# Optimization experiments

Hardware: AMD Instinct MI355X
Metric: run time of the kernel (lower is better)

The kernel has to match this reference:

```python
import jax, jax.numpy as jnp
import numpy as np

NEG_SLOPE = 0.2  # PyG GATConv default negative_slope


def setup_inputs() -> dict:
    key = jax.random.key(0)
    k1, k2, k3, k4, k5 = jax.random.split(key, 5)
    N, E, IN, H, C = 50000, 800000, 128, 4, 64
    x = jax.random.normal(k1, (N, IN), dtype=jnp.float32)
    edge_index = jax.random.randint(k2, (2, E), 0, N, dtype=jnp.int32)
    W = jax.random.normal(k3, (IN, H * C), dtype=jnp.float32) * (1.0 / np.sqrt(IN))
    att_src = jax.random.normal(k4, (H, C), dtype=jnp.float32) * 0.1
    att_dst = jax.random.normal(k5, (H, C), dtype=jnp.float32) * 0.1
    bias = jnp.zeros((C,), dtype=jnp.float32)
    return {"x": x, "edge_index": edge_index, "W": W,
            "att_src": att_src, "att_dst": att_dst, "bias": bias}


def reference(x, edge_index, W, att_src, att_dst, bias):
    N = x.shape[0]
    H, C = att_src.shape
    # add self loops (PyG GATConv default add_self_loops=True)
    loop = jnp.arange(N, dtype=edge_index.dtype)
    src = jnp.concatenate([edge_index[0], loop])  # message source j
    dst = jnp.concatenate([edge_index[1], loop])  # message target i
    # linear projection, per-head view [N, H, C]
    h = (x @ W).reshape(N, H, C)
    # per-node attention terms [N, H]
    a_src = jnp.einsum('nhc,hc->nh', h, att_src)
    a_dst = jnp.einsum('nhc,hc->nh', h, att_dst)
    # per-edge logits with leaky relu [Etot, H]
    e = jax.nn.leaky_relu(a_src[src] + a_dst[dst], NEG_SLOPE)
    # segment softmax over incoming edges of each destination node
    emax = jax.ops.segment_max(e, dst, num_segments=N)       # [N, H]
    ex = jnp.exp(e - emax[dst])                              # [Etot, H]
    denom = jax.ops.segment_sum(ex, dst, num_segments=N)     # [N, H]
    alpha = ex / denom[dst]                                  # [Etot, H]
    # weighted scatter-aggregate of source features
    msg = h[src] * alpha[:, :, None]                         # [Etot, H, C]
    out = jax.ops.segment_sum(msg, dst, num_segments=N)      # [N, H, C]
    # concat=False -> mean over heads, then bias, then module-level ELU
    out = out.mean(axis=1) + bias
    return jax.nn.elu(out)
```

## Files before the change

kernel.cpp:

```cpp
#include <hip/hip_runtime.h>

#define NEG_SLOPE 0.2f
static constexpr int IN_F = 128;
static constexpr int NHEAD = 4;
static constexpr int CH = 64;
static constexpr int HC = 256;
static constexpr int SC_EPB = 2000;
static constexpr int CB_CAP = 6144;
static constexpr int CPAD = 16;
static constexpr int PBC = 416;
static constexpr int PREPB = 128;

static __host__ size_t align256(size_t v) { return (v + 255) & ~((size_t)255); }

__device__ inline ushort f2bf(float f) {
    unsigned u = __float_as_uint(f);
    unsigned r = u + 0x7FFFu + ((u >> 16) & 1u);
    return (ushort)(r >> 16);
}
__device__ inline float bf2f(ushort s) { return __uint_as_float(((unsigned)s) << 16); }

typedef short s16x8 __attribute__((ext_vector_type(8)));
typedef float f32x16 __attribute__((ext_vector_type(16)));

__global__ __launch_bounds__(256) void prep_count_kernel(
    const float* __restrict__ W, ushort* __restrict__ Wt,
    const int* __restrict__ dst, int* __restrict__ ccnt,
    int* __restrict__ rowptr, int N, int Etot, int E, int epb, int NB)
{
    __shared__ int hist[256];
    int t = threadIdx.x;
    if (blockIdx.x < PREPB) {
        int f = blockIdx.x * 256 + t;
        int k = f >> 8;
        int n = f & 255;
        Wt[n * IN_F + k] = f2bf(W[(size_t)k * HC + n]);
        if (f == 0) rowptr[N] = Etot;
        return;
    }
    hist[t] = 0;
    __syncthreads();
    int slice = blockIdx.x - PREPB;
    int lo = slice * epb;
    int hi = min(E, lo + epb);
    for (int i = lo + t; i < hi; i += 256)
        atomicAdd(&hist[((unsigned)dst[i]) >> 8], 1);
    __syncthreads();
    if (t < NB && hist[t]) atomicAdd(&ccnt[t * CPAD], hist[t]);
}

__global__ __launch_bounds__(256) void bucket_scatter(
    const int* __restrict__ src, const int* __restrict__ dst,
    const int* __restrict__ ccnt, int* __restrict__ cur0,
    unsigned* __restrict__ ebuf, int E)
{
    __shared__ int eb[256];
    __shared__ int hist[256];
    __shared__ int lbase[256];
    __shared__ int gbase[256];
    __shared__ int cur[256];
    __shared__ unsigned sbuf[SC_EPB + 48];
    __shared__ unsigned char tb[SC_EPB + 48];
    int t = threadIdx.x;
    int cv = ccnt[t * CPAD];
    eb[t] = cv;
    __syncthreads();
    #pragma unroll
    for (int off = 1; off < 256; off <<= 1) {
        int a = eb[t];
        int b = (t >= off) ? eb[t - off] : 0;
        __syncthreads();
        eb[t] = a + b;
        __syncthreads();
    }
    int myebase = eb[t] - cv;
    __syncthreads();
    eb[t] = myebase;

    int lo = blockIdx.x * SC_EPB;
    int hi = min(E, lo + SC_EPB);
    int cnt = hi - lo;
    hist[t] = 0;
    __syncthreads();
    unsigned pk[8]; int bk[8];
    #pragma unroll
    for (int u = 0; u < 8; ++u) {
        int i = lo + t + 256 * u;
        bk[u] = -1;
        if (i < hi) {
            unsigned d = (unsigned)dst[i];
            bk[u] = (int)(d >> 8);
            pk[u] = (((unsigned)src[i]) << 8) | (d & 255u);
            atomicAdd(&hist[bk[u]], 1);
        }
    }
    __syncthreads();
    int v = hist[t];
    lbase[t] = v;
    __syncthreads();
    #pragma unroll
    for (int off = 1; off < 256; off <<= 1) {
        int a = lbase[t];
        int b = (t >= off) ? lbase[t - off] : 0;
        __syncthreads();
        lbase[t] = a + b;
        __syncthreads();
    }
    int excl = lbase[t] - v;
    if (v) gbase[t] = eb[t] + atomicAdd(&cur0[t * CPAD], v);
    __syncthreads();
    lbase[t] = excl;
    cur[t] = excl;
    __syncthreads();
    #pragma unroll
    for (int u = 0; u < 8; ++u) {
        if (bk[u] >= 0) {
            int p = atomicAdd(&cur[bk[u]], 1);
            sbuf[p] = pk[u];
            tb[p] = (unsigned char)bk[u];
        }
    }
    __syncthreads();
    for (int j = t; j < cnt; j += 256) {
        int b = tb[j];
        ebuf[gbase[b] + j - lbase[b]] = sbuf[j];
    }
}

__global__ __launch_bounds__(256) void gemm_csr_kernel(
    const float* __restrict__ x, const ushort* __restrict__ Wt,
    const float* __restrict__ att_src, const float* __restrict__ att_dst,
    ushort* __restrict__ hb, float* __restrict__ a_src, float* __restrict__ a_dst,
    const unsigned* __restrict__ ebuf, const int* __restrict__ ccnt,
    int* __restrict__ rowptr, int* __restrict__ csr_src,
    int NTB, int NB, int N)
{
    constexpr int LDK = 136;
    __shared__ __align__(16) char smem[64 * LDK * 2 + 128 * LDK * 2];
    const int t = threadIdx.x;

    if (blockIdx.x >= NTB) {
        int b = (blockIdx.x - NTB) * 2 + blockIdx.y;
        if (b >= NB) return;
        int* scn = (int*)smem;
        int* hist = (int*)(smem + 1024);
        int* cur = (int*)(smem + 2048);
        unsigned* srt = (unsigned*)(smem + 3072);
        int cv = ccnt[t * CPAD];
        scn[t] = cv;
        __syncthreads();
        #pragma unroll
        for (int off = 1; off < 256; off <<= 1) {
            int a = scn[t];
            int bb = (t >= off) ? scn[t - off] : 0;
            __syncthreads();
            scn[t] = a + bb;
            __syncthreads();
        }
        int lo = (b == 0) ? 0 : scn[b - 1];
        int hi = scn[b];
        __syncthreads();

        int n0 = b << 8;
        int ncnt = min(256, N - n0);
        int cnt = hi - lo;
        int cb = lo + n0;
        hist[t] = 0;
        __syncthreads();
        for (int i = lo + t; i < hi; i += 256)
            atomicAdd(&hist[ebuf[i] & 255u], 1);
        __syncthreads();
        int v = hist[t];
        scn[t] = v;
        __syncthreads();
        #pragma unroll
        for (int off = 1; off < 256; off <<= 1) {
            int a = scn[t];
            int bb = (t >= off) ? scn[t - off] : 0;
            __syncthreads();
            scn[t] = a + bb;
            __syncthreads();
        }
        int excl = scn[t] - v;
        if (t < ncnt) {
            int segstart = cb + excl + t;
            rowptr[n0 + t] = segstart;
            csr_src[segstart] = n0 + t;
        }
        cur[t] = excl;
        __syncthreads();
        if (cnt <= CB_CAP) {
            for (int i = lo + t; i < hi; i += 256) {
                unsigned e = ebuf[i];
                int p = atomicAdd(&cur[e & 255u], 1);
                srt[p] = e;
            }
            __syncthreads();
            for (int j = t; j < cnt; j += 256) {
                unsigned e = srt[j];
                csr_src[cb + j + (int)(e & 255u) + 1] = (int)(e >> 8);
            }
        } else {
            for (int i = lo + t; i < hi; i += 256) {
                unsigned e = ebuf[i];
                int ln = (int)(e & 255u);
                int p = atomicAdd(&cur[ln], 1);
                csr_src[cb + p + ln + 1] = (int)(e >> 8);
            }
        }
        return;
    }

    ushort* As = (ushort*)smem;
    ushort* Bs = (ushort*)(smem + 64 * LDK * 2);
    ushort* Hs = As;

    const int m0 = blockIdx.x * 64;
    const int n0 = blockIdx.y * 128;

    #pragma unroll
    for (int u = 0; u < 8; ++u) {
        int f = t + 256 * u;
        int r = f >> 5;
        int k4 = (f & 31) * 4;
        int row = m0 + r;
        float4 v = make_float4(0.f, 0.f, 0.f, 0.f);
        if (row < N) v = *(const float4*)(x + (size_t)row * IN_F + k4);
        ushort4 o;
        o.x = f2bf(v.x); o.y = f2bf(v.y); o.z = f2bf(v.z); o.w = f2bf(v.w);
        *(ushort4*)&As[r * LDK + k4] = o;
    }
    #pragma unroll
    for (int u = 0; u < 8; ++u) {
        int f = t + 256 * u;
        int n = f >> 4;
        int k8 = (f & 15) * 8;
        uint4 v = *(const uint4*)(Wt + (size_t)(n0 + n) * IN_F + k8);
        *(uint4*)&Bs[n * LDK + k8] = v;
    }
    __syncthreads();

    const int w = t >> 6;
    const int lane = t & 63;
    const int mrow = 32 * (w >> 1) + (lane & 31);
    const int nbase = 64 * (w & 1) + (lane & 31);
    const int kq = (lane >> 5) * 8;

    f32x16 acc0 = {}, acc1 = {};
    #pragma unroll
    for (int s = 0; s < 8; ++s) {
        s16x8 af = *(const s16x8*)&As[mrow * LDK + 16 * s + kq];
        s16x8 b0 = *(const s16x8*)&Bs[nbase * LDK + 16 * s + kq];
        s16x8 b1 = *(const s16x8*)&Bs[(nbase + 32) * LDK + 16 * s + kq];
        acc0 = __builtin_amdgcn_mfma_f32_32x32x16_bf16(af, b0, acc0, 0, 0, 0);
        acc1 = __builtin_amdgcn_mfma_f32_32x32x16_bf16(af, b1, acc1, 0, 0, 0);
    }
    __syncthreads();

    {
        int rbase = 4 * (lane >> 5) + 32 * (w >> 1);
        int c0 = 64 * (w & 1) + (lane & 31);
        #pragma unroll
        for (int r = 0; r < 16; ++r) {
            int rowL = rbase + (r & 3) + 8 * (r >> 2);
            Hs[rowL * LDK + c0]      = f2bf(acc0[r]);
            Hs[rowL * LDK + c0 + 32] = f2bf(acc1[r]);
        }
    }
    __syncthreads();

    {
        int r2 = t >> 2;
        int q = t & 3;
        int row = m0 + r2;
        uint4 p0 = *(const uint4*)&Hs[r2 * LDK + 32 * q];
        uint4 p1 = *(const uint4*)&Hs[r2 * LDK + 32 * q + 8];
        uint4 p2 = *(const uint4*)&Hs[r2 * LDK + 32 * q + 16];
        uint4 p3 = *(const uint4*)&Hs[r2 * LDK + 32 * q + 24];
        if (row < N) {
            ushort* dsth = hb + (size_t)row * HC + n0 + 32 * q;
            *(uint4*)(dsth)      = p0;
            *(uint4*)(dsth + 8)  = p1;
            *(uint4*)(dsth + 16) = p2;
            *(uint4*)(dsth + 24) = p3;
        }
        int hq = 2 * blockIdx.y + (q >> 1);
        int cb = (q & 1) * 32;
        const float* asp = att_src + hq * CH + cb;
        const float* adp = att_dst + hq * CH + cb;
        unsigned uu[16] = { p0.x, p0.y, p0.z, p0.w, p1.x, p1.y, p1.z, p1.w,
                            p2.x, p2.y, p2.z, p2.w, p3.x, p3.y, p3.z, p3.w };
        float ps = 0.f, pd = 0.f;
        #pragma unroll
        for (int i = 0; i < 16; ++i) {
            float lo = bf2f((ushort)(uu[i] & 0xFFFFu));
            float hi = bf2f((ushort)(uu[i] >> 16));
            ps += lo * asp[2 * i] + hi * asp[2 * i + 1];
            pd += lo * adp[2 * i] + hi * adp[2 * i + 1];
        }
        ps += __shfl_xor(ps, 1, 64);
        pd += __shfl_xor(pd, 1, 64);
        if ((q & 1) == 0 && row < N) {
            a_src[(size_t)row * NHEAD + hq] = ps;
            a_dst[(size_t)row * NHEAD + hq] = pd;
        }
    }
}

__global__ __launch_bounds__(256) void aggregate_kernel(
    const ushort* __restrict__ hb, const float* __restrict__ a_src,
    const float* __restrict__ a_dst, const int* __restrict__ rowptr,
    const int* __restrict__ csr_src, const float* __restrict__ bias,
    float* __restrict__ out, int N)
{
    int node = (int)((blockIdx.x * (size_t)blockDim.x + threadIdx.x) >> 6);
    int l = threadIdx.x & 63;
    if (node >= N) return;
    int start = rowptr[node];
    int end = rowptr[node + 1];
    int hd = l >> 4;
    float adh = a_dst[(size_t)node * NHEAD + hd];

    float4 acc0 = make_float4(0.f, 0.f, 0.f, 0.f);
    float4 acc1 = make_float4(0.f, 0.f, 0.f, 0.f);
    float4 acc2 = make_float4(0.f, 0.f, 0.f, 0.f);
    float4 acc3 = make_float4(0.f, 0.f, 0.f, 0.f);
    float s0 = 0.f, s1 = 0.f, s2 = 0.f, s3 = 0.f;

    int k = start;
    for (; k + 4 <= end; k += 4) {
        int sj0 = csr_src[k];
        int sj1 = csr_src[k + 1];
        int sj2 = csr_src[k + 2];
        int sj3 = csr_src[k + 3];
        float a0 = a_src[(size_t)sj0 * NHEAD + hd];
        float a1 = a_src[(size_t)sj1 * NHEAD + hd];
        float a2 = a_src[(size_t)sj2 * NHEAD + hd];
        float a3 = a_src[(size_t)sj3 * NHEAD + hd];
        ushort4 h0 = *(const ushort4*)(hb + ((size_t)sj0 << 8) + 4 * l);
        ushort4 h1 = *(const ushort4*)(hb + ((size_t)sj1 << 8) + 4 * l);
        ushort4 h2 = *(const ushort4*)(hb + ((size_t)sj2 << 8) + 4 * l);
        ushort4 h3 = *(const ushort4*)(hb + ((size_t)sj3 << 8) + 4 * l);
        float e0 = a0 + adh; e0 = fmaxf(e0, NEG_SLOPE * e0); float w0 = __expf(e0);
        float e1 = a1 + adh; e1 = fmaxf(e1, NEG_SLOPE * e1); float w1 = __expf(e1);
        float e2 = a2 + adh; e2 = fmaxf(e2, NEG_SLOPE * e2); float w2 = __expf(e2);
        float e3 = a3 + adh; e3 = fmaxf(e3, NEG_SLOPE * e3); float w3 = __expf(e3);
        s0 += w0; s1 += w1; s2 += w2; s3 += w3;
        acc0.x += w0 * bf2f(h0.x); acc0.y += w0 * bf2f(h0.y);
        acc0.z += w0 * bf2f(h0.z); acc0.w += w0 * bf2f(h0.w);
        acc1.x += w1 * bf2f(h1.x); acc1.y += w1 * bf2f(h1.y);
        acc1.z += w1 * bf2f(h1.z); acc1.w += w1 * bf2f(h1.w);
        acc2.x += w2 * bf2f(h2.x); acc2.y += w2 * bf2f(h2.y);
        acc2.z += w2 * bf2f(h2.z); acc2.w += w2 * bf2f(h2.w);
        acc3.x += w3 * bf2f(h3.x); acc3.y += w3 * bf2f(h3.y);
        acc3.z += w3 * bf2f(h3.z); acc3.w += w3 * bf2f(h3.w);
    }
    for (; k < end; ++k) {
        int sj0 = csr_src[k];
        float a0 = a_src[(size_t)sj0 * NHEAD + hd];
        ushort4 h0 = *(const ushort4*)(hb + ((size_t)sj0 << 8) + 4 * l);
        float e0 = a0 + adh; e0 = fmaxf(e0, NEG_SLOPE * e0);
        float w0 = __expf(e0);
        s0 += w0;
        acc0.x += w0 * bf2f(h0.x); acc0.y += w0 * bf2f(h0.y);
        acc0.z += w0 * bf2f(h0.z); acc0.w += w0 * bf2f(h0.w);
    }

    float inv = 1.0f / (s0 + s1 + s2 + s3);
    float4 acc;
    acc.x = (acc0.x + acc1.x + acc2.x + acc3.x) * inv;
    acc.y = (acc0.y + acc1.y + acc2.y + acc3.y) * inv;
    acc.z = (acc0.z + acc1.z + acc2.z + acc3.z) * inv;
    acc.w = (acc0.w + acc1.w + acc2.w + acc3.w) * inv;

    #pragma unroll
    for (int off = 16; off < 64; off <<= 1) {
        acc.x += __shfl_xor(acc.x, off, 64);
        acc.y += __shfl_xor(acc.y, off, 64);
        acc.z += __shfl_xor(acc.z, off, 64);
        acc.w += __shfl_xor(acc.w, off, 64);
    }
    if (l < 16) {
        float4 b4 = *(const float4*)(bias + 4 * l);
        float4 o;
        o.x = acc.x * 0.25f + b4.x;
        o.y = acc.y * 0.25f + b4.y;
        o.z = acc.z * 0.25f + b4.z;
        o.w = acc.w * 0.25f + b4.w;
        o.x = (o.x > 0.f) ? o.x : (__expf(o.x) - 1.f);
        o.y = (o.y > 0.f) ? o.y : (__expf(o.y) - 1.f);
        o.z = (o.z > 0.f) ? o.z : (__expf(o.z) - 1.f);
        o.w = (o.w > 0.f) ? o.w : (__expf(o.w) - 1.f);
        *(float4*)(out + (size_t)node * CH + 4 * l) = o;
    }
}

extern "C" void kernel_launch(void* const* d_in, const int* in_sizes, int n_in,
                              void* d_out, int out_size, void* d_ws, size_t ws_size,
                              hipStream_t stream)
{
    const float* x         = (const float*)d_in[0];
    const int*   edge_idx  = (const int*)d_in[1];
    const float* W         = (const float*)d_in[2];
    const float* att_src   = (const float*)d_in[3];
    const float* att_dst   = (const float*)d_in[4];
    const float* bias      = (const float*)d_in[5];
    float* out = (float*)d_out;

    const int N = in_sizes[0] / IN_F;
    const int E = in_sizes[1] / 2;
    const int Etot = E + N;
    const int NB = (N + 255) >> 8;
    const int* srcp = edge_idx;
    const int* dstp = edge_idx + E;

    char* ws = (char*)d_ws;
    size_t off = 0;
    ushort*  hb     = (ushort*)(ws + off);   off += align256((size_t)N * HC * sizeof(ushort));
    ushort*  Wt     = (ushort*)(ws + off);   off += align256((size_t)HC * IN_F * sizeof(ushort));
    float*   a_src  = (float*)(ws + off);    off += align256((size_t)N * NHEAD * sizeof(float));
    float*   a_dst  = (float*)(ws + off);    off += align256((size_t)N * NHEAD * sizeof(float));
    int*     ccnt   = (int*)(ws + off);      off += align256(256 * CPAD * sizeof(int));
    int*     cur0   = (int*)(ws + off);      off += align256(256 * CPAD * sizeof(int));
    unsigned* ebuf  = (unsigned*)(ws + off); off += align256((size_t)E * sizeof(unsigned));
    int*     rowptr = (int*)(ws + off);      off += align256(((size_t)N + 1) * sizeof(int));
    int*     csrs   = (int*)(ws + off);      off += align256((size_t)Etot * sizeof(int));
    (void)ws_size; (void)n_in; (void)out_size;

    const int NTB = (N + 63) / 64;
    const int epbc = (E + PBC - 1) / PBC;
    const int PBS = (E + SC_EPB - 1) / SC_EPB;
    const int NBH = (NB + 1) / 2;

    hipMemsetAsync(ccnt, 0, 2 * 256 * CPAD * sizeof(int), stream);
    prep_count_kernel<<<PREPB + PBC, 256, 0, stream>>>(
        W, Wt, dstp, ccnt, rowptr, N, Etot, E, epbc, NB);
    bucket_scatter<<<PBS, 256, 0, stream>>>(srcp, dstp, ccnt, cur0, ebuf, E);
    dim3 gg(NTB + NBH, 2);
    gemm_csr_kernel<<<gg, 256, 0, stream>>>(x, Wt, att_src, att_dst, hb,
                                            a_src, a_dst, ebuf, ccnt,
                                            rowptr, csrs, NTB, NB, N);
    aggregate_kernel<<<((size_t)N * 64 + 255) / 256, 256, 0, stream>>>(
        hb, a_src, a_dst, rowptr, csrs, bias, out, N);
}
```

Baseline: 206.9 us.

## Fuse prep, count, scatter, GEMM and CSR build into one cooperative kernel

Replaces the memset plus three preprocessing launches with a single persistent cooperative kernel that steps through the phases separated by grid-wide syncs. Each block loops over its share of the jobs in every phase. This removes the launch gaps and the memset, and the GEMM now reads B fragments straight from global Wt instead of staging them in LDS. The risk is the cost of the grid syncs and lower occupancy from the launch_bounds hint. A fallback path with separate kernels runs if the cooperative launch fails.

```diff
diff --git a/kernel.cpp b/kernel.cpp
--- a/kernel.cpp
+++ b/kernel.cpp
@@ -1,4 +1,6 @@
 #include <hip/hip_runtime.h>
+#include <hip/hip_cooperative_groups.h>
+namespace cg = cooperative_groups;
 
 #define NEG_SLOPE 0.2f
 static constexpr int IN_F = 128;
@@ -9,7 +11,6 @@
 static constexpr int CB_CAP = 6144;
 static constexpr int CPAD = 16;
 static constexpr int PBC = 416;
-static constexpr int PREPB = 128;
 
 static __host__ size_t align256(size_t v) { return (v + 255) & ~((size_t)255); }
 
@@ -23,33 +24,296 @@
 typedef short s16x8 __attribute__((ext_vector_type(8)));
 typedef float f32x16 __attribute__((ext_vector_type(16)));
 
-__global__ __launch_bounds__(256) void prep_count_kernel(
+__global__ __launch_bounds__(256, 4) void fused_prep_kernel(
+    const float* __restrict__ x, const float* __restrict__ W,
+    ushort* __restrict__ Wt,
+    const float* __restrict__ att_src, const float* __restrict__ att_dst,
+    ushort* __restrict__ hb, float* __restrict__ a_src, float* __restrict__ a_dst,
+    const int* __restrict__ src, const int* __restrict__ dst,
+    int* __restrict__ ccnt, int* __restrict__ cur0,
+    unsigned* __restrict__ ebuf, int* __restrict__ rowptr, int* __restrict__ csr_src,
+    int N, int E, int Etot, int NB, int NTB, int epbc, int PBS)
+{
+    constexpr int LDK = 136;
+    __shared__ __align__(16) char smem[27648];
+    __shared__ int ebs[257];
+    cg::grid_group grd = cg::this_grid();
+    const int t = threadIdx.x;
+    const int gsz = gridDim.x * 256;
+    const int gtid = blockIdx.x * 256 + t;
+
+    for (int i = gtid; i < 256 * CPAD; i += gsz) { ccnt[i] = 0; cur0[i] = 0; }
+    for (int f = gtid; f < IN_F * HC; f += gsz) {
+        int k = f >> 8, n = f & 255;
+        Wt[n * IN_F + k] = f2bf(W[(size_t)k * HC + n]);
+    }
+    if (gtid == 0) rowptr[N] = Etot;
+    __threadfence();
+    grd.sync();
+
+    {
+        int* hist = (int*)smem;
+        for (int job = blockIdx.x; job < PBC; job += gridDim.x) {
+            __syncthreads();
+            hist[t] = 0;
+            __syncthreads();
+            int lo = job * epbc, hi = min(E, lo + epbc);
+            for (int i = lo + t; i < hi; i += 256)
+                atomicAdd(&hist[((unsigned)dst[i]) >> 8], 1);
+            __syncthreads();
+            if (t < NB && hist[t]) atomicAdd(&ccnt[t * CPAD], hist[t]);
+        }
+    }
+    __threadfence();
+    grd.sync();
+
+    {
+        int* scn = (int*)smem;
+        int cv = ccnt[t * CPAD];
+        scn[t] = cv;
+        __syncthreads();
+        #pragma unroll
+        for (int off = 1; off < 256; off <<= 1) {
+            int a = scn[t];
+            int b = (t >= off) ? scn[t - off] : 0;
+            __syncthreads();
+            scn[t] = a + b;
+            __syncthreads();
+        }
+        ebs[t] = scn[t] - cv;
+        if (t == 255) ebs[256] = scn[255];
+        __syncthreads();
+
+        int* hist  = (int*)smem;
+        int* lbase = (int*)(smem + 1024);
+        int* gbase = (int*)(smem + 2048);
+        int* cur   = (int*)(smem + 3072);
+        unsigned* sbuf = (unsigned*)(smem + 4096);
+        unsigned char* tb = (unsigned char*)(smem + 4096 + (SC_EPB + 48) * 4);
+        for (int job = blockIdx.x; job < PBS; job += gridDim.x) {
+            __syncthreads();
+            hist[t] = 0;
+            __syncthreads();
+            int lo = job * SC_EPB;
+            int hi = min(E, lo + SC_EPB);
+            int cnt = hi - lo;
+            unsigned pk[8]; int bk[8];
+            #pragma unroll
+            for (int u = 0; u < 8; ++u) {
+                int i = lo + t + 256 * u;
+                bk[u] = -1;
+                if (i < hi) {
+                    unsigned d = (unsigned)dst[i];
+                    bk[u] = (int)(d >> 8);
+                    pk[u] = (((unsigned)src[i]) << 8) | (d & 255u);
+                    atomicAdd(&hist[bk[u]], 1);
+                }
+            }
+            __syncthreads();
+            int v = hist[t];
+            lbase[t] = v;
+            __syncthreads();
+            #pragma unroll
+            for (int off = 1; off < 256; off <<= 1) {
+                int a = lbase[t];
+                int b = (t >= off) ? lbase[t - off] : 0;
+                __syncthreads();
+                lbase[t] = a + b;
+                __syncthreads();
+            }
+            int excl = lbase[t] - v;
+            if (v) gbase[t] = ebs[t] + atomicAdd(&cur0[t * CPAD], v);
+            __syncthreads();
+            lbase[t] = excl;
+            cur[t] = excl;
+            __syncthreads();
+            #pragma unroll
+            for (int u = 0; u < 8; ++u) {
+                if (bk[u] >= 0) {
+                    int p = atomicAdd(&cur[bk[u]], 1);
+                    sbuf[p] = pk[u];
+                    tb[p] = (unsigned char)bk[u];
+                }
+            }
+            __syncthreads();
+            for (int j = t; j < cnt; j += 256) {
+                int b = tb[j];
+                ebuf[gbase[b] + j - lbase[b]] = sbuf[j];
+            }
+        }
+    }
+    __threadfence();
+    grd.sync();
+
+    {
+        int njobs = NTB * 2 + NB;
+        for (int job = blockIdx.x; job < njobs; job += gridDim.x) {
+            __syncthreads();
+            if (job < NTB * 2) {
+                ushort* As = (ushort*)smem;
+                int m0 = (job >> 1) * 64;
+                int jy = job & 1;
+                int n0 = jy * 128;
+                #pragma unroll
+                for (int u = 0; u < 8; ++u) {
+                    int f = t + 256 * u;
+                    int r = f >> 5;
+                    int k4 = (f & 31) * 4;
+                    int row = m0 + r;
+                    float4 v = make_float4(0.f, 0.f, 0.f, 0.f);
+                    if (row < N) v = *(const float4*)(x + (size_t)row * IN_F + k4);
+                    ushort4 o;
+                    o.x = f2bf(v.x); o.y = f2bf(v.y); o.z = f2bf(v.z); o.w = f2bf(v.w);
+                    *(ushort4*)&As[r * LDK + k4] = o;
+                }
+                __syncthreads();
+                int w = t >> 6, lane = t & 63;
+                int mrow = 32 * (w >> 1) + (lane & 31);
+                int nbg = n0 + 64 * (w & 1) + (lane & 31);
+                int kq = (lane >> 5) * 8;
+                f32x16 acc0 = {}, acc1 = {};
+                #pragma unroll
+                for (int s = 0; s < 8; ++s) {
+                    s16x8 af = *(const s16x8*)&As[mrow * LDK + 16 * s + kq];
+                    s16x8 b0 = *(const s16x8*)(Wt + (size_t)nbg * IN_F + 16 * s + kq);
+                    s16x8 b1 = *(const s16x8*)(Wt + (size_t)(nbg + 32) * IN_F + 16 * s + kq);
+                    acc0 = __builtin_amdgcn_mfma_f32_32x32x16_bf16(af, b0, acc0, 0, 0, 0);
+                    acc1 = __builtin_amdgcn_mfma_f32_32x32x16_bf16(af, b1, acc1, 0, 0, 0);
+                }
+                __syncthreads();
+                ushort* Hs = As;
+                {
+                    int rbase = 4 * (lane >> 5) + 32 * (w >> 1);
+                    int c0 = 64 * (w & 1) + (lane & 31);
+                    #pragma unroll
+                    for (int r = 0; r < 16; ++r) {
+                        int rowL = rbase + (r & 3) + 8 * (r >> 2);
+                        Hs[rowL * LDK + c0]      = f2bf(acc0[r]);
+                        Hs[rowL * LDK + c0 + 32] = f2bf(acc1[r]);
+                    }
+                }
+                __syncthreads();
+                {
+                    int r2 = t >> 2;
+                    int q = t & 3;
+                    int row = m0 + r2;
+                    uint4 p0 = *(const uint4*)&Hs[r2 * LDK + 32 * q];
+                    uint4 p1 = *(const uint4*)&Hs[r2 * LDK + 32 * q + 8];
+                    uint4 p2 = *(const uint4*)&Hs[r2 * LDK + 32 * q + 16];
+                    uint4 p3 = *(const uint4*)&Hs[r2 * LDK + 32 * q + 24];
+                    if (row < N) {
+                        ushort* dsth = hb + (size_t)row * HC + n0 + 32 * q;
+                        *(uint4*)(dsth)      = p0;
+                        *(uint4*)(dsth + 8)  = p1;
+                        *(uint4*)(dsth + 16) = p2;
+                        *(uint4*)(dsth + 24) = p3;
+                    }
+                    int hq = 2 * jy + (q >> 1);
+                    int cb = (q & 1) * 32;
+                    const float* asp = att_src + hq * CH + cb;
+                    const float* adp = att_dst + hq * CH + cb;
+                    unsigned uu[16] = { p0.x, p0.y, p0.z, p0.w, p1.x, p1.y, p1.z, p1.w,
+                                        p2.x, p2.y, p2.z, p2.w, p3.x, p3.y, p3.z, p3.w };
+                    float ps = 0.f, pd = 0.f;
+                    #pragma unroll
+                    for (int i = 0; i < 16; ++i) {
+                        float lo = bf2f((ushort)(uu[i] & 0xFFFFu));
+                        float hi = bf2f((ushort)(uu[i] >> 16));
+                        ps += lo * asp[2 * i] + hi * asp[2 * i + 1];
+                        pd += lo * adp[2 * i] + hi * adp[2 * i + 1];
+                    }
+                    ps += __shfl_xor(ps, 1, 64);
+                    pd += __shfl_xor(pd, 1, 64);
+                    if ((q & 1) == 0 && row < N) {
+                        a_src[(size_t)row * NHEAD + hq] = ps;
+                        a_dst[(size_t)row * NHEAD + hq] = pd;
+                    }
+                }
+            } else {
+                int b = job - NTB * 2;
+                int* scn = (int*)smem;
+                int* hist = (int*)(smem + 1024);
+                int* cur = (int*)(smem + 2048);
+                unsigned* srt = (unsigned*)(smem + 3072);
+                int lo = ebs[b], hi = ebs[b + 1];
+                int n0 = b << 8;
+                int ncnt = min(256, N - n0);
+                int cnt = hi - lo;
+                int cb = lo + n0;
+                hist[t] = 0;
+                __syncthreads();
+                for (int i = lo + t; i < hi; i += 256)
+                    atomicAdd(&hist[ebuf[i] & 255u], 1);
+                __syncthreads();
+                int v = hist[t];
+                scn[t] = v;
+                __syncthreads();
+                #pragma unroll
+                for (int off = 1; off < 256; off <<= 1) {
+                    int a = scn[t];
+                    int bb = (t >= off) ? scn[t - off] : 0;
+                    __syncthreads();
+                    scn[t] = a + bb;
+                    __syncthreads();
+                }
+                int excl = scn[t] - v;
+                if (t < ncnt) {
+                    int seg = cb + excl + t;
+                    rowptr[n0 + t] = seg;
+                    csr_src[seg] = n0 + t;
+                }
+                cur[t] = excl;
+                __syncthreads();
+                if (cnt <= CB_CAP) {
+                    for (int i = lo + t; i < hi; i += 256) {
+                        unsigned e = ebuf[i];
+                        int p = atomicAdd(&cur[e & 255u], 1);
+                        srt[p] = e;
+                    }
+                    __syncthreads();
+                    for (int j = t; j < cnt; j += 256) {
+                        unsigned e = srt[j];
+                        csr_src[cb + j + (int)(e & 255u) + 1] = (int)(e >> 8);
+                    }
+                } else {
+                    for (int i = lo + t; i < hi; i += 256) {
+                        unsigned e = ebuf[i];
+                        int ln = (int)(e & 255u);
+                        int p = atomicAdd(&cur[ln], 1);
+                        csr_src[cb + p + ln + 1] = (int)(e >> 8);
+                    }
+                }
+            }
+        }
+    }
+}
+
+__global__ __launch_bounds__(256) void fb_prep_count(
     const float* __restrict__ W, ushort* __restrict__ Wt,
-    const int* __restrict__ dst, int* __restrict__ ccnt,
+    const int* __restrict__ dst, int* __restrict__ ccnt, int* __restrict__ cur0,
     int* __restrict__ rowptr, int N, int Etot, int E, int epb, int NB)
 {
     __shared__ int hist[256];
     int t = threadIdx.x;
-    if (blockIdx.x < PREPB) {
+    if (blockIdx.x < 128) {
         int f = blockIdx.x * 256 + t;
-        int k = f >> 8;
-        int n = f & 255;
+        int k = f >> 8, n = f & 255;
         Wt[n * IN_F + k] = f2bf(W[(size_t)k * HC + n]);
+        if (f < 256 * CPAD) { ccnt[f] = 0; cur0[f] = 0; }
         if (f == 0) rowptr[N] = Etot;
         return;
     }
     hist[t] = 0;
     __syncthreads();
-    int slice = blockIdx.x - PREPB;
-    int lo = slice * epb;
-    int hi = min(E, lo + epb);
+    int slice = blockIdx.x - 128;
+    int lo = slice * epb, hi = min(E, lo + epb);
     for (int i = lo + t; i < hi; i += 256)
         atomicAdd(&hist[((unsigned)dst[i]) >> 8], 1);
     __syncthreads();
     if (t < NB && hist[t]) atomicAdd(&ccnt[t * CPAD], hist[t]);
 }
 
-__global__ __launch_bounds__(256) void bucket_scatter(
+__global__ __launch_bounds__(256) void fb_scatter(
     const int* __restrict__ src, const int* __restrict__ dst,
     const int* __restrict__ ccnt, int* __restrict__ cur0,
     unsigned* __restrict__ ebuf, int E)
@@ -73,10 +337,9 @@
         eb[t] = a + b;
         __syncthreads();
     }
-    int myebase = eb[t] - cv;
-    __syncthreads();
-    eb[t] = myebase;
-
+    int myeb = eb[t] - cv;
+    __syncthreads();
+    eb[t] = myeb;
     int lo = blockIdx.x * SC_EPB;
     int hi = min(E, lo + SC_EPB);
     int cnt = hi - lo;
@@ -127,7 +390,7 @@
     }
 }
 
-__global__ __launch_bounds__(256) void gemm_csr_kernel(
+__global__ __launch_bounds__(256) void fb_gemm_csr(
     const float* __restrict__ x, const ushort* __restrict__ Wt,
     const float* __restrict__ att_src, const float* __restrict__ att_dst,
     ushort* __restrict__ hb, float* __restrict__ a_src, float* __restrict__ a_dst,
@@ -136,11 +399,10 @@
     int NTB, int NB, int N)
 {
     constexpr int LDK = 136;
-    __shared__ __align__(16) char smem[64 * LDK * 2 + 128 * LDK * 2];
+    __shared__ __align__(16) char smem[27648];
     const int t = threadIdx.x;
-
-    if (blockIdx.x >= NTB) {
-        int b = (blockIdx.x - NTB) * 2 + blockIdx.y;
+    if (blockIdx.x >= NTB * 2) {
+        int b = blockIdx.x - NTB * 2;
         if (b >= NB) return;
         int* scn = (int*)smem;
         int* hist = (int*)(smem + 1024);
@@ -160,7 +422,6 @@
         int lo = (b == 0) ? 0 : scn[b - 1];
         int hi = scn[b];
         __syncthreads();
-
         int n0 = b << 8;
         int ncnt = min(256, N - n0);
         int cnt = hi - lo;
@@ -183,9 +444,9 @@
         }
         int excl = scn[t] - v;
         if (t < ncnt) {
-            int segstart = cb + excl + t;
-            rowptr[n0 + t] = segstart;
-            csr_src[segstart] = n0 + t;
+            int seg = cb + excl + t;
+            rowptr[n0 + t] = seg;
+            csr_src[seg] = n0 + t;
         }
         cur[t] = excl;
         __syncthreads();
@@ -210,14 +471,10 @@
         }
         return;
     }
-
     ushort* As = (ushort*)smem;
-    ushort* Bs = (ushort*)(smem + 64 * LDK * 2);
-    ushort* Hs = As;
-
-    const int m0 = blockIdx.x * 64;
-    const int n0 = blockIdx.y * 128;
-
+    int m0 = (blockIdx.x >> 1) * 64;
+    int jy = blockIdx.x & 1;
+    int n0 = jy * 128;
     #pragma unroll
     for (int u = 0; u < 8; ++u) {
         int f = t + 256 * u;
@@ -230,33 +487,22 @@
         o.x = f2bf(v.x); o.y = f2bf(v.y); o.z = f2bf(v.z); o.w = f2bf(v.w);
         *(ushort4*)&As[r * LDK + k4] = o;
     }
-    #pragma unroll
-    for (int u = 0; u < 8; ++u) {
-        int f = t + 256 * u;
-        int n = f >> 4;
-        int k8 = (f & 15) * 8;
-        uint4 v = *(const uint4*)(Wt + (size_t)(n0 + n) * IN_F + k8);
-        *(uint4*)&Bs[n * LDK + k8] = v;
-    }
-    __syncthreads();
-
-    const int w = t >> 6;
-    const int lane = t & 63;
-    const int mrow = 32 * (w >> 1) + (lane & 31);
-    const int nbase = 64 * (w & 1) + (lane & 31);
-    const int kq = (lane >> 5) * 8;
-
+    __syncthreads();
+    int w = t >> 6, lane = t & 63;
+    int mrow = 32 * (w >> 1) + (lane & 31);
+    int nbg = n0 + 64 * (w & 1) + (lane & 31);
+    int kq = (lane >> 5) * 8;
     f32x16 acc0 = {}, acc1 = {};
     #pragma unroll
     for (int s = 0; s < 8; ++s) {
         s16x8 af = *(const s16x8*)&As[mrow * LDK + 16 * s + kq];
-        s16x8 b0 = *(const s16x8*)&Bs[nbase * LDK + 16 * s + kq];
-        s16x8 b1 = *(const s16x8*)&Bs[(nbase + 32) * LDK + 16 * s + kq];
+        s16x8 b0 = *(const s16x8*)(Wt + (size_t)nbg * IN_F + 16 * s + kq);
+        s16x8 b1 = *(const s16x8*)(Wt + (size_t)(nbg + 32) * IN_F + 16 * s + kq);
         acc0 = __builtin_amdgcn_mfma_f32_32x32x16_bf16(af, b0, acc0, 0, 0, 0);
         acc1 = __builtin_amdgcn_mfma_f32_32x32x16_bf16(af, b1, acc1, 0, 0, 0);
     }
     __syncthreads();
-
+    ushort* Hs = As;
     {
         int rbase = 4 * (lane >> 5) + 32 * (w >> 1);
         int c0 = 64 * (w & 1) + (lane & 31);
@@ -268,7 +514,6 @@
         }
     }
     __syncthreads();
-
     {
         int r2 = t >> 2;
         int q = t & 3;
@@ -284,7 +529,7 @@
             *(uint4*)(dsth + 16) = p2;
             *(uint4*)(dsth + 24) = p3;
         }
-        int hq = 2 * blockIdx.y + (q >> 1);
+        int hq = 2 * jy + (q >> 1);
         int cb = (q & 1) * 32;
         const float* asp = att_src + hq * CH + cb;
         const float* adp = att_dst + hq * CH + cb;
@@ -407,10 +652,10 @@
     const float* bias      = (const float*)d_in[5];
     float* out = (float*)d_out;
 
-    const int N = in_sizes[0] / IN_F;
-    const int E = in_sizes[1] / 2;
-    const int Etot = E + N;
-    const int NB = (N + 255) >> 8;
+    int N = in_sizes[0] / IN_F;
+    int E = in_sizes[1] / 2;
+    int Etot = E + N;
+    int NB = (N + 255) >> 8;
     const int* srcp = edge_idx;
     const int* dstp = edge_idx + E;
 
@@ -427,19 +672,45 @@
     int*     csrs   = (int*)(ws + off);      off += align256((size_t)Etot * sizeof(int));
     (void)ws_size; (void)n_in; (void)out_size;
 
-    const int NTB = (N + 63) / 64;
-    const int epbc = (E + PBC - 1) / PBC;
-    const int PBS = (E + SC_EPB - 1) / SC_EPB;
-    const int NBH = (NB + 1) / 2;
-
-    hipMemsetAsync(ccnt, 0, 2 * 256 * CPAD * sizeof(int), stream);
-    prep_count_kernel<<<PREPB + PBC, 256, 0, stream>>>(
-        W, Wt, dstp, ccnt, rowptr, N, Etot, E, epbc, NB);
-    bucket_scatter<<<PBS, 256, 0, stream>>>(srcp, dstp, ccnt, cur0, ebuf, E);
-    dim3 gg(NTB + NBH, 2);
-    gemm_csr_kernel<<<gg, 256, 0, stream>>>(x, Wt, att_src, att_dst, hb,
-                                            a_src, a_dst, ebuf, ccnt,
-                                            rowptr, csrs, NTB, NB, N);
+    int NTB = (N + 63) / 64;
+    int epbc = (E + PBC - 1) / PBC;
+    int PBS = (E + SC_EPB - 1) / SC_EPB;
+
+    int nbpc = 0;
+    hipOccupancyMaxActiveBlocksPerMultiprocessor(&nbpc, fused_prep_kernel, 256, 0);
+    if (nbpc < 1) nbpc = 1;
+    int ncu = 256;
+    hipDeviceProp_t prop;
+    int dev = 0;
+    if (hipGetDevice(&dev) == hipSuccess &&
+        hipGetDeviceProperties(&prop, dev) == hipSuccess)
+        ncu = prop.multiProcessorCount;
+    int grid = nbpc * ncu;
+    int maxjobs = NTB * 2 + NB;
+    if (grid > maxjobs) grid = maxjobs;
+
+    void* args[] = {
+        (void*)&x, (void*)&W, (void*)&Wt, (void*)&att_src, (void*)&att_dst,
+        (void*)&hb, (void*)&a_src, (void*)&a_dst, (void*)&srcp, (void*)&dstp,
+        (void*)&ccnt, (void*)&cur0, (void*)&ebuf, (void*)&rowptr, (void*)&csrs,
+        (void*)&N, (void*)&E, (void*)&Etot, (void*)&NB, (void*)&NTB,
+        (void*)&epbc, (void*)&PBS
+    };
+    hipError_t cerr = hipLaunchCooperativeKernel(
+        (const void*)fused_prep_kernel, dim3(grid), dim3(256), args, 0, stream);
+
+    if (cerr != hipSuccess) {
+        hipMemsetAsync(ccnt, 0, 256 * CPAD * sizeof(int), stream);
+        hipMemsetAsync(cur0, 0, 256 * CPAD * sizeof(int), stream);
+        int epbf = (E + PBC - 1) / PBC;
+        fb_prep_count<<<128 + PBC, 256, 0, stream>>>(
+            W, Wt, dstp, ccnt, cur0, rowptr, N, Etot, E, epbf, NB);
+        fb_scatter<<<PBS, 256, 0, stream>>>(srcp, dstp, ccnt, cur0, ebuf, E);
+        fb_gemm_csr<<<NTB * 2 + NB, 256, 0, stream>>>(
+            x, Wt, att_src, att_dst, hb, a_src, a_dst, ebuf, ccnt,
+            rowptr, csrs, NTB, NB, N);
+    }
+
     aggregate_kernel<<<((size_t)N * 64 + 255) / 256, 256, 0, stream>>>(
         hb, a_src, a_dst, rowptr, csrs, bias, out, N);
 }
```

New measurement: 482.3 us. 2.33x slower.
